# Kernel tuning notes

Measured on AMD Instinct MI355X. Metric: run time of the kernel, lower is better.

The kernel has to match this reference:

```python
import jax, jax.numpy as jnp
import numpy as np
import math

SAMPLE_RATE = 16000
CUTOFF = 7500.0
Q = 0.707  # torchaudio default for lowpass_biquad

def _lowpass_biquad_coeffs(sample_rate, cutoff_freq, Q):
    w0 = 2.0 * math.pi * cutoff_freq / sample_rate
    alpha = math.sin(w0) / (2.0 * Q)
    cos_w0 = math.cos(w0)
    b0 = (1.0 - cos_w0) / 2.0
    b1 = 1.0 - cos_w0
    b2 = b0
    a0 = 1.0 + alpha
    a1 = -2.0 * cos_w0
    a2 = 1.0 - alpha
    # normalize by a0 (as torchaudio's biquad/lfilter does)
    return (b0 / a0, b1 / a0, b2 / a0, a1 / a0, a2 / a0)


def setup_inputs() -> dict:
    key = jax.random.key(0)
    x = jax.random.normal(key, (64, 320000), dtype=jnp.float32)
    return {"x": x}


def reference(x) -> jnp.ndarray:
    b0, b1, b2, a1, a2 = _lowpass_biquad_coeffs(SAMPLE_RATE, CUTOFF, Q)
    b0 = jnp.asarray(b0, x.dtype); b1 = jnp.asarray(b1, x.dtype)
    b2 = jnp.asarray(b2, x.dtype); a1 = jnp.asarray(a1, x.dtype)
    a2 = jnp.asarray(a2, x.dtype)

    B = x.shape[0]
    xT = jnp.swapaxes(x, 0, 1)  # [T, B] -> scan over time

    def step(carry, xn):
        x1, x2, y1, y2 = carry  # each [B]
        yn = b0 * xn + b1 * x1 + b2 * x2 - a1 * y1 - a2 * y2
        return (xn, x1, yn, y1), yn

    z = jnp.zeros((B,), x.dtype)
    _, yT = jax.lax.scan(step, (z, z, z, z), xT)
    return jnp.swapaxes(yT, 0, 1)  # [B, T]
```

## Files before the change

kernel.cpp:

```cpp
#include <hip/hip_runtime.h>
#include <cmath>

#ifndef M_PI
#define M_PI 3.14159265358979323846
#endif

constexpr int T_LEN  = 320000;
constexpr int B_ROWS = 64;
constexpr int CHUNK  = 32;
constexpr int WARM   = 64;
constexpr int NCHUNK = T_LEN / CHUNK;
constexpr int BLK_CHUNKS = 256;
constexpr int BLK_SPAN   = BLK_CHUNKS * CHUNK;
constexpr int TILE_VECS  = (BLK_SPAN + WARM) / 4;
constexpr int WARM_VECS  = WARM / 4;
constexpr int VPT        = CHUNK / 4;

__device__ __forceinline__ int swzv(int V) { return V ^ ((V >> 3) & 7); }

__global__ __launch_bounds__(256, 4) void biquad_lds_kernel(
    const float* __restrict__ x, float* __restrict__ y,
    float b0, float b1, float b2, float a1, float a2) {
  const int b   = blockIdx.x;
  const int row = blockIdx.y;
  const int t   = threadIdx.x;

  const int S       = b * BLK_SPAN;
  const int nchunks = min(BLK_CHUNKS, (T_LEN - S) / CHUNK);
  const int nvecs   = nchunks * VPT;

  const float* xr = x + (size_t)row * T_LEN;
  float*       yr = y + (size_t)row * T_LEN;

  __shared__ float4 lds4[TILE_VECS];

  if (b == 0) {
    if (t < WARM_VECS) lds4[swzv(t)] = make_float4(0.f, 0.f, 0.f, 0.f);
    const float4* src = reinterpret_cast<const float4*>(xr);
    for (int i = t; i < nvecs; i += 256) lds4[swzv(WARM_VECS + i)] = src[i];
  } else {
    const float4* src = reinterpret_cast<const float4*>(xr + S - WARM);
    const int nf4 = nvecs + WARM_VECS;
    for (int i = t; i < nf4; i += 256) lds4[swzv(i)] = src[i];
  }
  __syncthreads();

  const bool active = (t < nchunks);
  float4 m[VPT];
  float x1 = 0.f, x2 = 0.f, y1 = 0.f, y2 = 0.f;

  auto step = [&](float xn) -> float {
    float tt = fmaf(b2, x2, fmaf(b1, x1, b0 * xn));
    float u  = fmaf(-a2, y2, tt);
    float yn = fmaf(-a1, y1, u);
    x2 = x1; x1 = xn;
    y2 = y1; y1 = yn;
    return yn;
  };

  if (active) {
    const int vb = t * VPT;
#pragma unroll
    for (int g = 0; g < WARM_VECS / 4; ++g) {
      float4 w0 = lds4[swzv(vb + g * 4 + 0)];
      float4 w1 = lds4[swzv(vb + g * 4 + 1)];
      float4 w2 = lds4[swzv(vb + g * 4 + 2)];
      float4 w3 = lds4[swzv(vb + g * 4 + 3)];
      step(w0.x); step(w0.y); step(w0.z); step(w0.w);
      step(w1.x); step(w1.y); step(w1.z); step(w1.w);
      step(w2.x); step(w2.y); step(w2.z); step(w2.w);
      step(w3.x); step(w3.y); step(w3.z); step(w3.w);
    }
#pragma unroll
    for (int k = 0; k < VPT; ++k) m[k] = lds4[swzv(vb + WARM_VECS + k)];
#pragma unroll
    for (int k = 0; k < VPT; ++k) {
      float4 v = m[k];
      m[k] = make_float4(step(v.x), step(v.y), step(v.z), step(v.w));
    }
  }
  __syncthreads();

  if (active) {
    const int ob = t * VPT + WARM_VECS;
#pragma unroll
    for (int k = 0; k < VPT; ++k) lds4[swzv(ob + k)] = m[k];
  }
  __syncthreads();

  {
    float4* dst = reinterpret_cast<float4*>(yr + S);
    for (int i = t; i < nvecs; i += 256) dst[i] = lds4[swzv(WARM_VECS + i)];
  }
}

extern "C" void kernel_launch(void* const* d_in, const int* in_sizes, int n_in,
                              void* d_out, int out_size, void* d_ws, size_t ws_size,
                              hipStream_t stream) {
  const float* x = (const float*)d_in[0];
  float*       y = (float*)d_out;

  const double sample_rate = 16000.0, cutoff = 7500.0, Q = 0.707;
  double w0    = 2.0 * M_PI * cutoff / sample_rate;
  double alpha = sin(w0) / (2.0 * Q);
  double cw    = cos(w0);
  double a0    = 1.0 + alpha;
  float b0 = (float)(((1.0 - cw) * 0.5) / a0);
  float b1 = (float)((1.0 - cw) / a0);
  float b2 = b0;
  float a1 = (float)((-2.0 * cw) / a0);
  float a2 = (float)((1.0 - alpha) / a0);

  dim3 block(256);
  dim3 grid((NCHUNK + BLK_CHUNKS - 1) / BLK_CHUNKS, B_ROWS);
  hipLaunchKernelGGL(biquad_lds_kernel, grid, block, 0, stream,
                     x, y, b0, b1, b2, a1, a2);
}
```

Baseline: 33.36 us.

## Replace warm-up recomputation with zero-state chunk scan plus homogeneous-response combine

Each thread previously ran 64 warm-up samples before its 32-sample chunk, relying on the filter's decay to approximate the incoming state. Now each thread filters its chunk from zero state and publishes its final state. A combine step then composes three preceding chunk states using precomputed impulse-response coefficients and adds the homogeneous correction to each output. This cuts the serial work per thread from 96 steps to roughly 32 plus a short correction pass, at the cost of extra shared memory, a longer correction chain, and truncating the state propagation to three chunks.

```diff
diff --git a/kernel.cpp b/kernel.cpp
--- a/kernel.cpp
+++ b/kernel.cpp
@@ -8,19 +8,20 @@
 constexpr int T_LEN  = 320000;
 constexpr int B_ROWS = 64;
 constexpr int CHUNK  = 32;
-constexpr int WARM   = 64;
+constexpr int VPT    = CHUNK / 4;
 constexpr int NCHUNK = T_LEN / CHUNK;
 constexpr int BLK_CHUNKS = 256;
 constexpr int BLK_SPAN   = BLK_CHUNKS * CHUNK;
-constexpr int TILE_VECS  = (BLK_SPAN + WARM) / 4;
-constexpr int WARM_VECS  = WARM / 4;
-constexpr int VPT        = CHUNK / 4;
+constexpr int HALO       = 3;
+constexpr int HALO_VECS  = HALO * VPT;
+constexpr int TILE_VECS  = HALO_VECS + BLK_CHUNKS * VPT;
 
 __device__ __forceinline__ int swzv(int V) { return V ^ ((V >> 3) & 7); }
 
-__global__ __launch_bounds__(256, 4) void biquad_lds_kernel(
+__global__ __launch_bounds__(256, 4) void biquad_combine_kernel(
     const float* __restrict__ x, float* __restrict__ y,
-    float b0, float b1, float b2, float a1, float a2) {
+    float b0, float b1, float b2, float a1, float a2,
+    float q30, float p30, float q31, float p31) {
   const int b   = blockIdx.x;
   const int row = blockIdx.y;
   const int t   = threadIdx.x;
@@ -32,65 +33,97 @@
   const float* xr = x + (size_t)row * T_LEN;
   float*       yr = y + (size_t)row * T_LEN;
 
-  __shared__ float4 lds4[TILE_VECS];
+  __shared__ float4 tile[TILE_VECS];
+  __shared__ float4 st[HALO + BLK_CHUNKS];
 
   if (b == 0) {
-    if (t < WARM_VECS) lds4[swzv(t)] = make_float4(0.f, 0.f, 0.f, 0.f);
     const float4* src = reinterpret_cast<const float4*>(xr);
-    for (int i = t; i < nvecs; i += 256) lds4[swzv(WARM_VECS + i)] = src[i];
+    for (int i = t; i < HALO_VECS + nvecs; i += 256)
+      tile[swzv(i)] = (i < HALO_VECS) ? make_float4(0.f, 0.f, 0.f, 0.f)
+                                      : src[i - HALO_VECS];
   } else {
-    const float4* src = reinterpret_cast<const float4*>(xr + S - WARM);
-    const int nf4 = nvecs + WARM_VECS;
-    for (int i = t; i < nf4; i += 256) lds4[swzv(i)] = src[i];
+    const float4* src = reinterpret_cast<const float4*>(xr + S - HALO * CHUNK);
+    for (int i = t; i < HALO_VECS + nvecs; i += 256) tile[swzv(i)] = src[i];
   }
   __syncthreads();
 
-  const bool active = (t < nchunks);
-  float4 m[VPT];
-  float x1 = 0.f, x2 = 0.f, y1 = 0.f, y2 = 0.f;
-
-  auto step = [&](float xn) -> float {
-    float tt = fmaf(b2, x2, fmaf(b1, x1, b0 * xn));
-    float u  = fmaf(-a2, y2, tt);
-    float yn = fmaf(-a1, y1, u);
-    x2 = x1; x1 = xn;
-    y2 = y1; y1 = yn;
+  auto stepf = [&](float xn, float& X1, float& X2, float& Y1, float& Y2) -> float {
+    float tt = fmaf(b2, X2, fmaf(b1, X1, b0 * xn));
+    float u  = fmaf(-a2, Y2, tt);
+    float yn = fmaf(-a1, Y1, u);
+    X2 = X1; X1 = xn;
+    Y2 = Y1; Y1 = yn;
     return yn;
   };
 
+  if (t < HALO) {
+    float4 h[VPT];
+#pragma unroll
+    for (int k = 0; k < VPT; ++k) h[k] = tile[swzv(t * VPT + k)];
+    float hxl1 = h[VPT - 1].w, hxl2 = h[VPT - 1].z;
+    float hx1 = 0.f, hx2 = 0.f, hy1 = 0.f, hy2 = 0.f;
+#pragma unroll
+    for (int k = 0; k < VPT; ++k) {
+      stepf(h[k].x, hx1, hx2, hy1, hy2); stepf(h[k].y, hx1, hx2, hy1, hy2);
+      stepf(h[k].z, hx1, hx2, hy1, hy2); stepf(h[k].w, hx1, hx2, hy1, hy2);
+    }
+    st[t] = make_float4(hy1, hy2, hxl1, hxl2);
+  }
+
+  const bool active = (t < nchunks);
+  float4 m[VPT];
+  const int vb = HALO_VECS + t * VPT;
   if (active) {
-    const int vb = t * VPT;
 #pragma unroll
-    for (int g = 0; g < WARM_VECS / 4; ++g) {
-      float4 w0 = lds4[swzv(vb + g * 4 + 0)];
-      float4 w1 = lds4[swzv(vb + g * 4 + 1)];
-      float4 w2 = lds4[swzv(vb + g * 4 + 2)];
-      float4 w3 = lds4[swzv(vb + g * 4 + 3)];
-      step(w0.x); step(w0.y); step(w0.z); step(w0.w);
-      step(w1.x); step(w1.y); step(w1.z); step(w1.w);
-      step(w2.x); step(w2.y); step(w2.z); step(w2.w);
-      step(w3.x); step(w3.y); step(w3.z); step(w3.w);
-    }
-#pragma unroll
-    for (int k = 0; k < VPT; ++k) m[k] = lds4[swzv(vb + WARM_VECS + k)];
+    for (int k = 0; k < VPT; ++k) m[k] = tile[swzv(vb + k)];
+    float xl1 = m[VPT - 1].w, xl2 = m[VPT - 1].z;
+    float x1 = 0.f, x2 = 0.f, y1 = 0.f, y2 = 0.f;
 #pragma unroll
     for (int k = 0; k < VPT; ++k) {
       float4 v = m[k];
-      m[k] = make_float4(step(v.x), step(v.y), step(v.z), step(v.w));
+      m[k] = make_float4(stepf(v.x, x1, x2, y1, y2), stepf(v.y, x1, x2, y1, y2),
+                         stepf(v.z, x1, x2, y1, y2), stepf(v.w, x1, x2, y1, y2));
     }
+    st[HALO + t] = make_float4(y1, y2, xl1, xl2);
   }
   __syncthreads();
 
   if (active) {
-    const int ob = t * VPT + WARM_VECS;
+    const int i = HALO + t;
+    float4 sm3 = st[i - 3], sm2 = st[i - 2], sm1 = st[i - 1];
+    float cA0 = fmaf(b1, sm3.z, fmaf(b2, sm3.w, fmaf(-a1, sm3.x, -a2 * sm3.y)));
+    float cA1 = fmaf(-a1, cA0, fmaf(b2, sm3.z, -a2 * sm3.x));
+    float yA1 = fmaf(q31, cA0, fmaf(p31, cA1, sm2.x));
+    float yA2 = fmaf(q30, cA0, fmaf(p30, cA1, sm2.y));
+    float cB0 = fmaf(b1, sm2.z, fmaf(b2, sm2.w, fmaf(-a1, yA1, -a2 * yA2)));
+    float cB1 = fmaf(-a1, cB0, fmaf(b2, sm2.z, -a2 * yA1));
+    float yB1 = fmaf(q31, cB0, fmaf(p31, cB1, sm1.x));
+    float yB2 = fmaf(q30, cB0, fmaf(p30, cB1, sm1.y));
+    float c0 = fmaf(b1, sm1.z, fmaf(b2, sm1.w, fmaf(-a1, yB1, -a2 * yB2)));
+    float c1 = fmaf(-a1, c0, fmaf(b2, sm1.z, -a2 * yB1));
+    float cm2, cm1;
+    {
+      m[0].x += c0; m[0].y += c1;
+      float c2 = fmaf(-a1, c1, -a2 * c0); m[0].z += c2;
+      float c3 = fmaf(-a1, c2, -a2 * c1); m[0].w += c3;
+      cm2 = c2; cm1 = c3;
+    }
 #pragma unroll
-    for (int k = 0; k < VPT; ++k) lds4[swzv(ob + k)] = m[k];
+    for (int k = 1; k < VPT; ++k) {
+      float ca = fmaf(-a1, cm1, -a2 * cm2); m[k].x += ca;
+      float cb = fmaf(-a1, ca, -a2 * cm1);  m[k].y += cb;
+      float cc = fmaf(-a1, cb, -a2 * ca);   m[k].z += cc;
+      float cd = fmaf(-a1, cc, -a2 * cb);   m[k].w += cd;
+      cm2 = cc; cm1 = cd;
+    }
+#pragma unroll
+    for (int k = 0; k < VPT; ++k) tile[swzv(vb + k)] = m[k];
   }
   __syncthreads();
 
   {
     float4* dst = reinterpret_cast<float4*>(yr + S);
-    for (int i = t; i < nvecs; i += 256) dst[i] = lds4[swzv(WARM_VECS + i)];
+    for (int i = t; i < nvecs; i += 256) dst[i] = tile[swzv(HALO_VECS + i)];
   }
 }
 
@@ -105,14 +138,24 @@
   double alpha = sin(w0) / (2.0 * Q);
   double cw    = cos(w0);
   double a0    = 1.0 + alpha;
-  float b0 = (float)(((1.0 - cw) * 0.5) / a0);
-  float b1 = (float)((1.0 - cw) / a0);
-  float b2 = b0;
-  float a1 = (float)((-2.0 * cw) / a0);
-  float a2 = (float)((1.0 - alpha) / a0);
+  double b0d = ((1.0 - cw) * 0.5) / a0;
+  double b1d = (1.0 - cw) / a0;
+  double a1d = (-2.0 * cw) / a0;
+  double a2d = (1.0 - alpha) / a0;
+
+  double qm2 = 1.0, pm2 = 0.0, qm1 = 0.0, pm1 = 1.0;
+  double q30 = 0, p30 = 0, q31 = 0, p31 = 0;
+  for (int n = 2; n < CHUNK; ++n) {
+    double qn = -a1d * qm1 - a2d * qm2;
+    double pn = -a1d * pm1 - a2d * pm2;
+    qm2 = qm1; pm2 = pm1; qm1 = qn; pm1 = pn;
+    if (n == 30) { q30 = qn; p30 = pn; }
+    if (n == 31) { q31 = qn; p31 = pn; }
+  }
 
   dim3 block(256);
   dim3 grid((NCHUNK + BLK_CHUNKS - 1) / BLK_CHUNKS, B_ROWS);
-  hipLaunchKernelGGL(biquad_lds_kernel, grid, block, 0, stream,
-                     x, y, b0, b1, b2, a1, a2);
+  hipLaunchKernelGGL(biquad_combine_kernel, grid, block, 0, stream,
+                     x, y, (float)b0d, (float)b1d, (float)b0d, (float)a1d, (float)a2d,
+                     (float)q30, (float)p30, (float)q31, (float)p31);
 }
```

Measured after the change: 33.87 us. Within noise of the previous version (+1.5%).
